# Optimization experiments

Hardware: AMD Instinct MI355X
Metric: run time of the kernel (lower is better)

The kernel has to match this reference:

```python
import jax, jax.numpy as jnp
import numpy as np

B, C, N = 8, 256, 4096
CQK = C // 4  # 64
BN_EPS = 1e-5


def setup_inputs() -> dict:
    key = jax.random.key(0)
    ks = jax.random.split(key, 10)
    s = 1.0 / np.sqrt(C)
    return {
        "x": jax.random.normal(ks[0], (B, C, N), jnp.float32),
        "xyz": jax.random.normal(ks[1], (B, C, N), jnp.float32),
        # q_conv and k_conv share the same weight/bias in the original module
        "wqk": jax.random.uniform(ks[2], (CQK, C), jnp.float32, -s, s),
        "bqk": jax.random.uniform(ks[3], (CQK,), jnp.float32, -s, s),
        "wv": jax.random.uniform(ks[4], (C, C), jnp.float32, -s, s),
        "bv": jax.random.uniform(ks[5], (C,), jnp.float32, -s, s),
        "wt": jax.random.uniform(ks[6], (C, C), jnp.float32, -s, s),
        "bt": jax.random.uniform(ks[7], (C,), jnp.float32, -s, s),
        "bn_gamma": jnp.ones((C,), jnp.float32),
        "bn_beta": jnp.zeros((C,), jnp.float32),
        "bn_mean": jax.random.normal(ks[8], (C,), jnp.float32) * 0.1,
        "bn_var": jax.random.uniform(ks[9], (C,), jnp.float32, 0.5, 1.5),
    }


def _conv1x1(x, w, b):
    # x: [B, Cin, N], w: [Cout, Cin], b: [Cout] -> [B, Cout, N]
    return jnp.einsum('oc,bcn->bon', w, x) + b[None, :, None]


def reference(x, xyz, wqk, bqk, wv, bv, wt, bt, bn_gamma, bn_beta, bn_mean, bn_var):
    x = x + xyz
    q = _conv1x1(x, wqk, bqk)            # [B, 64, N]
    k = _conv1x1(x, wqk, bqk)            # [B, 64, N] (shared weights)
    v = _conv1x1(x, wv, bv)              # [B, C, N]
    energy = jnp.einsum('bci,bcj->bij', q, k)   # q^T k -> [B, N, N]
    attn = jax.nn.softmax(energy, axis=-1)
    attn = attn / (1e-9 + attn.sum(axis=1, keepdims=True))  # L1 column renorm
    x_r = jnp.einsum('bcn,bnm->bcm', v, attn)    # [B, C, N]
    t = _conv1x1(x - x_r, wt, bt)
    # BatchNorm1d (eval mode, running stats)
    inv = jax.lax.rsqrt(bn_var + BN_EPS)
    t = (t - bn_mean[None, :, None]) * (inv * bn_gamma)[None, :, None] + bn_beta[None, :, None]
    x_r = jnp.where(t >= 0, t, 0.2 * t)          # LeakyReLU(0.2)
    return x + x_r
```

## Files before the change

### kernel.cpp

```cpp
#include <hip/hip_runtime.h>
#include <math.h>

#define B_   8
#define C_   256
#define N_   4096
#define CQK_ 64
#define JS_  8
#define NSPLIT 2
#define NRANGE (N_ / NSPLIT)

#define SCQ 1.20110674f
#define THR2 11.54f

typedef __attribute__((ext_vector_type(8))) short short8v;
typedef __attribute__((ext_vector_type(4))) short short4v;
typedef __attribute__((ext_vector_type(4))) float f32x4;
typedef __attribute__((ext_vector_type(16))) float f32x16;
typedef __attribute__((ext_vector_type(4))) unsigned int uint4v;

__device__ __forceinline__ unsigned short f2bf(float f) {
    unsigned u = __float_as_uint(f);
    u += 0x7fffu + ((u >> 16) & 1u);
    return (unsigned short)(u >> 16);
}
__device__ __forceinline__ float bf2f(unsigned short h) {
    return __uint_as_float((unsigned)h << 16);
}


__global__ __launch_bounds__(256) void wcvt_kernel(const float* __restrict__ wqk,
                                                   const float* __restrict__ wv,
                                                   const float* __restrict__ wt,
                                                   unsigned short* __restrict__ wh) {
    int i = (blockIdx.x * 256 + threadIdx.x) * 4;
    const float* src; int off;
    if (i < 16384)      { src = wqk; off = i; }
    else if (i < 81920) { src = wv;  off = i - 16384; }
    else                { src = wt;  off = i - 81920; }
    float4 v = *(const float4*)(src + off);
    short4v o;
    o[0] = (short)f2bf(v.x); o[1] = (short)f2bf(v.y);
    o[2] = (short)f2bf(v.z); o[3] = (short)f2bf(v.w);
    *(short4v*)(wh + i) = o;
}

__global__ __launch_bounds__(256) void addt_kernel(const float* __restrict__ x,
                                                   const float* __restrict__ xyz,
                                                   float* __restrict__ xs,
                                                   unsigned short* __restrict__ xst) {
    __shared__ float st[64][65];
    const int tid = threadIdx.x;
    const int n0 = blockIdx.x * 64, c0 = blockIdx.y * 64, b = blockIdx.z;
    const size_t base = ((size_t)b * C_ + c0) * N_ + n0;
#pragma unroll
    for (int r = 0; r < 4; ++r) {
        int c = r * 16 + (tid >> 4);
        int nc = (tid & 15) * 4;
        size_t off = base + (size_t)c * N_ + nc;
        float4 xv = *(const float4*)(x + off);
        float4 yv = *(const float4*)(xyz + off);
        float4 s = make_float4(xv.x + yv.x, xv.y + yv.y, xv.z + yv.z, xv.w + yv.w);
        *(float4*)(xs + off) = s;
        st[c][nc] = s.x; st[c][nc + 1] = s.y; st[c][nc + 2] = s.z; st[c][nc + 3] = s.w;
    }
    __syncthreads();
    int n = tid >> 2, cc = (tid & 3) * 16;
    short8v p0, p1;
#pragma unroll
    for (int j = 0; j < 8; ++j) {
        p0[j] = (short)f2bf(st[cc + j][n]);
        p1[j] = (short)f2bf(st[cc + 8 + j][n]);
    }
    size_t ob = ((size_t)b * N_ + n0 + n) * 256 + c0 + cc;
    *(short8v*)(xst + ob) = p0;
    *(short8v*)(xst + ob + 8) = p1;
}

__global__ __launch_bounds__(256, 4) void convq_kernel(const unsigned short* __restrict__ xst,
                                                       const unsigned short* __restrict__ wh,
                                                       const float* __restrict__ bias,
                                                       unsigned short* __restrict__ Qf) {
    const int tid = threadIdx.x, wave = tid >> 6, lane = tid & 63, q = lane & 15, g = lane >> 4;
    const int n0 = blockIdx.x * 64, b = blockIdx.y;
    const unsigned short* xb = xst + (size_t)b * N_ * 256;
    f32x4 acc[4];
#pragma unroll
    for (int j = 0; j < 4; ++j) acc[j] = (f32x4){0.f, 0.f, 0.f, 0.f};
    for (int ks = 0; ks < 8; ++ks) {
        short8v aw = *(const short8v*)(wh + (size_t)(wave * 16 + q) * 256 + ks * 32 + 8 * g);
#pragma unroll
        for (int j = 0; j < 4; ++j) {
            short8v bx = *(const short8v*)(xb + (size_t)(n0 + j * 16 + q) * 256 + ks * 32 + 8 * g);
            acc[j] = __builtin_amdgcn_mfma_f32_16x16x32_bf16(aw, bx, acc[j], 0, 0, 0);
        }
    }
#pragma unroll
    for (int j = 0; j < 4; ++j) {
        short4v pk;
#pragma unroll
        for (int r = 0; r < 4; ++r)
            pk[r] = (short)f2bf((acc[j][r] + bias[wave * 16 + 4 * g + r]) * SCQ);
        const int n = n0 + j * 16 + q;
        size_t a = ((((size_t)b * 128 + (n >> 5)) * 4 + wave) * 64 + (g >> 1) * 32 + (n & 31)) * 8
                   + (g & 1) * 4;
        *(short4v*)(Qf + a) = pk;
    }
}

__global__ __launch_bounds__(512, 2) void convv_kernel(const unsigned short* __restrict__ xst,
                                                       const unsigned short* __restrict__ wh,
                                                       const float* __restrict__ bias,
                                                       const float* __restrict__ rsinv,
                                                       unsigned short* __restrict__ Vf) {
    const int tid = threadIdx.x, wave = tid >> 6, lane = tid & 63, q = lane & 15, g = lane >> 4;
    const int n0 = blockIdx.x * 64, o0 = blockIdx.y * 128, b = blockIdx.z;
    const int oo = o0 + wave * 16;
    const unsigned short* xb = xst + (size_t)b * N_ * 256;
    const float* rsb = rsinv + (size_t)b * N_;
    f32x4 acc[4];
#pragma unroll
    for (int j = 0; j < 4; ++j) acc[j] = (f32x4){0.f, 0.f, 0.f, 0.f};
    for (int ks = 0; ks < 8; ++ks) {
        short8v bw = *(const short8v*)(wh + (size_t)(oo + q) * 256 + ks * 32 + 8 * g);
#pragma unroll
        for (int j = 0; j < 4; ++j) {
            short8v ax = *(const short8v*)(xb + (size_t)(n0 + j * 16 + q) * 256 + ks * 32 + 8 * g);
            acc[j] = __builtin_amdgcn_mfma_f32_16x16x32_bf16(ax, bw, acc[j], 0, 0, 0);
        }
    }
    float bo = bias[oo + q];
    const int c = oo + q;
#pragma unroll
    for (int j = 0; j < 4; ++j) {
        f32x4 rs4 = *(const f32x4*)(rsb + n0 + j * 16 + 4 * g);
        short4v pk;
#pragma unroll
        for (int r = 0; r < 4; ++r) pk[r] = (short)f2bf((acc[j][r] + bo) * rs4[r]);
        size_t a = ((((size_t)b * 256 + (n0 >> 4) + j) * 8 + (c >> 5)) * 64
                    + (g >> 1) * 32 + (c & 31)) * 8 + (g & 1) * 4;
        *(short4v*)(Vf + a) = pk;
    }
}

__global__ __launch_bounds__(256) void rowstats_mfma(const unsigned short* __restrict__ Qf,
                                                     float* __restrict__ pmax,
                                                     float* __restrict__ psum) {
    const int tid = threadIdx.x;
    const int wave = tid >> 6, lane = tid & 63, l31 = lane & 31;
    const int bid = blockIdx.x;
    const int b  = bid & 7;
    const int it = (bid >> 3) & 31;
    const int js = bid >> 8;
    const int i0 = it * 128 + wave * 32;
    const unsigned short* Qb = Qf + (size_t)b * 128 * 4 * 512;

    short8v bqi[4];
#pragma unroll
    for (int ks = 0; ks < 4; ++ks)
        bqi[ks] = *(const short8v*)(Qb + (((size_t)(i0 >> 5) * 4 + ks) * 64 + lane) * 8);

    float m = -1e30f, s = 0.f;
    const int jbeg = js * (N_ / JS_);
    for (int j0 = jbeg; j0 < jbeg + N_ / JS_; j0 += 32) {
        short8v an[4];
#pragma unroll
        for (int ks = 0; ks < 4; ++ks)
            an[ks] = *(const short8v*)(Qb + (((size_t)(j0 >> 5) * 4 + ks) * 64 + lane) * 8);
        f32x16 e;
#pragma unroll
        for (int r = 0; r < 16; ++r) e[r] = 0.f;
#pragma unroll
        for (int ks = 0; ks < 4; ++ks)
            e = __builtin_amdgcn_mfma_f32_32x32x16_bf16(an[ks], bqi[ks], e, 0, 0, 0);
        float pm = e[0];
#pragma unroll
        for (int r = 1; r < 16; ++r) pm = fmaxf(pm, e[r]);
        if (!__all(pm <= m + THR2)) {
            float mn = fmaxf(m, pm);
            s *= exp2f(m - mn);
            m = mn;
        }
#pragma unroll
        for (int r = 0; r < 16; ++r) s += exp2f(e[r] - m);
    }
    {
        float mo = __shfl_xor(m, 32);
        float so = __shfl_xor(s, 32);
        float mn = fmaxf(m, mo);
        s = s * exp2f(m - mn) + so * exp2f(mo - mn);
        m = mn;
    }
    if (lane < 32) {
        size_t o = ((size_t)js * B_ + b) * N_ + i0 + l31;
        pmax[o] = m;
        psum[o] = s;
    }
}

__global__ __launch_bounds__(256) void rowmerge_kernel(const float* __restrict__ pmax,
                                                       const float* __restrict__ psum,
                                                       float* __restrict__ rmneg,
                                                       float* __restrict__ rsinv) {
    size_t i = (size_t)blockIdx.x * 256 + threadIdx.x;
    float m = -1e30f;
#pragma unroll
    for (int js = 0; js < JS_; ++js) m = fmaxf(m, pmax[(size_t)js * B_ * N_ + i]);
    float s = 0.f;
#pragma unroll
    for (int js = 0; js < JS_; ++js)
        s += psum[(size_t)js * B_ * N_ + i] * exp2f(pmax[(size_t)js * B_ * N_ + i] - m);
    rmneg[i] = -m;
    rsinv[i] = 1.f / s;
}

__global__ __launch_bounds__(256, 2) void pv_mfma32(const unsigned short* __restrict__ Qf,
                                                    const unsigned short* __restrict__ Vf,
                                                    const float* __restrict__ rmneg,
                                                    const float* __restrict__ rsinv,
                                                    unsigned short* __restrict__ pxr,
                                                    float* __restrict__ pcs) {
    const int tid = threadIdx.x;
    const int wave = tid >> 6, lane = tid & 63, l31 = lane & 31, hi = lane >> 5;
    const int bid = blockIdx.x;
    const int b  = bid & 7;
    const int mc = (bid >> 3) & 31;
    const int ns = bid >> 8;
    const int m0 = mc * 128 + wave * 32;
    const int nbeg = ns * NRANGE;
    const unsigned short* Qb = Qf + (size_t)b * 128 * 4 * 512;
    const unsigned short* Vb = Vf + (size_t)b * 256 * 8 * 512;
    const float* rmb = rmneg + (size_t)b * N_;
    const float* rsb = rsinv + (size_t)b * N_;

    short8v bqm[4];
#pragma unroll
    for (int ks = 0; ks < 4; ++ks)
        bqm[ks] = *(const short8v*)(Qb + (((size_t)(m0 >> 5) * 4 + ks) * 64 + lane) * 8);

    f32x16 acc[8];
#pragma unroll
    for (int cb = 0; cb < 8; ++cb)
#pragma unroll
        for (int r = 0; r < 16; ++r) acc[cb][r] = 0.f;
    f32x4 csum4 = {0.f, 0.f, 0.f, 0.f};

#pragma unroll 1
    for (int it = 0; it < NRANGE / 32; ++it) {
        const int n0 = nbeg + it * 32;
        const int nt = n0 >> 5;
        short8v an[4];
#pragma unroll
        for (int ks = 0; ks < 4; ++ks)
            an[ks] = *(const short8v*)(Qb + (((size_t)nt * 4 + ks) * 64 + lane) * 8);
        f32x4 rmn[4], rs[4];
#pragma unroll
        for (int s = 0; s < 4; ++s) {
            rmn[s] = *(const f32x4*)(rmb + n0 + 8 * s + 4 * hi);
            rs[s]  = *(const f32x4*)(rsb + n0 + 8 * s + 4 * hi);
        }
        f32x16 e;
#pragma unroll
        for (int s = 0; s < 4; ++s) {
            e[4 * s + 0] = rmn[s][0]; e[4 * s + 1] = rmn[s][1];
            e[4 * s + 2] = rmn[s][2]; e[4 * s + 3] = rmn[s][3];
        }
#pragma unroll
        for (int ks = 0; ks < 4; ++ks)
            e = __builtin_amdgcn_mfma_f32_32x32x16_bf16(an[ks], bqm[ks], e, 0, 0, 0);
        unsigned dw[8];
#pragma unroll
        for (int s = 0; s < 4; ++s) {
            float p0 = exp2f(e[4 * s + 0]);
            float p1 = exp2f(e[4 * s + 1]);
            float p2 = exp2f(e[4 * s + 2]);
            float p3 = exp2f(e[4 * s + 3]);
            csum4[s] += (p0 * rs[s][0] + p1 * rs[s][1]) + (p2 * rs[s][2] + p3 * rs[s][3]);
            asm("v_cvt_pk_bf16_f32 %0, %1, %2" : "=v"(dw[2 * s + 0]) : "v"(p0), "v"(p1));
            asm("v_cvt_pk_bf16_f32 %0, %1, %2" : "=v"(dw[2 * s + 1]) : "v"(p2), "v"(p3));
        }
        asm("v_permlane32_swap_b32 %0, %1" : "+v"(dw[0]), "+v"(dw[2]));
        asm("v_permlane32_swap_b32 %0, %1" : "+v"(dw[1]), "+v"(dw[3]));
        asm("v_permlane32_swap_b32 %0, %1" : "+v"(dw[4]), "+v"(dw[6]));
        asm("v_permlane32_swap_b32 %0, %1" : "+v"(dw[5]), "+v"(dw[7]));
        uint4v t0 = {dw[0], dw[1], dw[2], dw[3]};
        uint4v t1 = {dw[4], dw[5], dw[6], dw[7]};
        short8v pf0 = __builtin_bit_cast(short8v, t0);
        short8v pf1 = __builtin_bit_cast(short8v, t1);
        const size_t vb0 = (size_t)(nt * 2) * 8;
#pragma unroll
        for (int cb = 0; cb < 8; ++cb) {
            short8v v0 = *(const short8v*)(Vb + ((vb0 + cb) * 64 + lane) * 8);
            acc[cb] = __builtin_amdgcn_mfma_f32_32x32x16_bf16(v0, pf0, acc[cb], 0, 0, 0);
        }
#pragma unroll
        for (int cb = 0; cb < 8; ++cb) {
            short8v v1 = *(const short8v*)(Vb + ((vb0 + 8 + cb) * 64 + lane) * 8);
            acc[cb] = __builtin_amdgcn_mfma_f32_32x32x16_bf16(v1, pf1, acc[cb], 0, 0, 0);
        }
    }

    float csum = (csum4[0] + csum4[1]) + (csum4[2] + csum4[3]);
    csum += __shfl_xor(csum, 32);
    if (lane < 32) pcs[((size_t)ns * B_ + b) * N_ + m0 + lane] = csum;
    unsigned short* pb = pxr + ((size_t)ns * B_ + b) * N_ * 256;
    const int m = m0 + l31;
#pragma unroll
    for (int cb = 0; cb < 8; ++cb)
#pragma unroll
        for (int s = 0; s < 4; ++s) {
            short4v pk;
#pragma unroll
            for (int r = 0; r < 4; ++r) pk[r] = (short)f2bf(acc[cb][4 * s + r]);
            *(short4v*)(pb + (size_t)m * 256 + cb * 32 + 8 * s + 4 * hi) = pk;
        }
}

__global__ __launch_bounds__(256) void reduce_diff(const unsigned short* __restrict__ pxr,
                                                   const float* __restrict__ pcs,
                                                   unsigned short* __restrict__ dh) {
    size_t i = (size_t)blockIdx.x * 256 + threadIdx.x;
    size_t e0 = i * 8;
    int m = (int)((e0 >> 8) & (N_ - 1));
    int b = (int)(e0 >> 20);
    float cs = pcs[(size_t)b * N_ + m] + pcs[((size_t)B_ + b) * N_ + m];
    float inv = 1.f / (1e-9f + cs);
    short8v p0 = *(const short8v*)(pxr + e0);
    short8v p1 = *(const short8v*)(pxr + (size_t)B_ * N_ * 256 + e0);
    short8v xv = *(const short8v*)(dh + e0);
    short8v o;
#pragma unroll
    for (int j = 0; j < 8; ++j) {
        float xr = (bf2f((unsigned short)p0[j]) + bf2f((unsigned short)p1[j])) * inv;
        o[j] = (short)f2bf(bf2f((unsigned short)xv[j]) - xr);
    }
    *(short8v*)(dh + e0) = o;
}

__global__ __launch_bounds__(512, 2) void convt_kernel(const unsigned short* __restrict__ dh,
                                                       const unsigned short* __restrict__ wh,
                                                       const float* __restrict__ bt,
                                                       const float* __restrict__ xs,
                                                       float* __restrict__ out,
                                                       const float* __restrict__ gam,
                                                       const float* __restrict__ bet,
                                                       const float* __restrict__ mu,
                                                       const float* __restrict__ var) {
    const int tid = threadIdx.x, wave = tid >> 6, lane = tid & 63, q = lane & 15, g = lane >> 4;
    const int m0 = blockIdx.x * 64, c0 = blockIdx.y * 128, b = blockIdx.z;
    const int cc = c0 + wave * 16;
    const unsigned short* db = dh + (size_t)b * N_ * 256;
    f32x4 acc[4];
#pragma unroll
    for (int j = 0; j < 4; ++j) acc[j] = (f32x4){0.f, 0.f, 0.f, 0.f};
    for (int ks = 0; ks < 8; ++ks) {
        short8v bw = *(const short8v*)(wh + (size_t)(cc + q) * 256 + ks * 32 + 8 * g);
#pragma unroll
        for (int j = 0; j < 4; ++j) {
            short8v ad = *(const short8v*)(db + (size_t)(m0 + j * 16 + q) * 256 + ks * 32 + 8 * g);
            acc[j] = __builtin_amdgcn_mfma_f32_16x16x32_bf16(ad, bw, acc[j], 0, 0, 0);
        }
    }
    const int c = cc + q;
    const float sc = rsqrtf(var[c] + 1e-5f) * gam[c];
    const float sh = bet[c] - mu[c] * sc;
    const float bb = bt[c];
#pragma unroll
    for (int j = 0; j < 4; ++j) {
        size_t off = ((size_t)b * C_ + c) * N_ + m0 + j * 16 + 4 * g;
        float4 xv = *(const float4*)(xs + off);
        float4 o;
        float tn;
        tn = (acc[j][0] + bb) * sc + sh; o.x = xv.x + (tn >= 0.f ? tn : 0.2f * tn);
        tn = (acc[j][1] + bb) * sc + sh; o.y = xv.y + (tn >= 0.f ? tn : 0.2f * tn);
        tn = (acc[j][2] + bb) * sc + sh; o.z = xv.z + (tn >= 0.f ? tn : 0.2f * tn);
        tn = (acc[j][3] + bb) * sc + sh; o.w = xv.w + (tn >= 0.f ? tn : 0.2f * tn);
        *(float4*)(out + off) = o;
    }
}

extern "C" void kernel_launch(void* const* d_in, const int* in_sizes, int n_in,
                              void* d_out, int out_size, void* d_ws, size_t ws_size,
                              hipStream_t stream) {
    (void)in_sizes; (void)n_in; (void)out_size; (void)ws_size;
    const float* x   = (const float*)d_in[0];
    const float* xyz = (const float*)d_in[1];
    const float* wqk = (const float*)d_in[2];
    const float* bqk = (const float*)d_in[3];
    const float* wv  = (const float*)d_in[4];
    const float* bv  = (const float*)d_in[5];
    const float* wt  = (const float*)d_in[6];
    const float* bt  = (const float*)d_in[7];
    const float* gam = (const float*)d_in[8];
    const float* bet = (const float*)d_in[9];
    const float* mu  = (const float*)d_in[10];
    const float* var = (const float*)d_in[11];
    float* out = (float*)d_out;

    const size_t M8 = (size_t)B_ * C_ * N_;
    float* ws = (float*)d_ws;
    size_t off = 0;
    float* xs = ws + off;                              off += M8;
    unsigned short* xst = (unsigned short*)(ws + off); off += M8 / 2;
    unsigned short* Qf  = (unsigned short*)(ws + off); off += M8 / 8;
    unsigned short* Vf  = (unsigned short*)(ws + off); off += M8 / 2;
    unsigned short* wh  = (unsigned short*)(ws + off); off += 81920;
    float* pmax = ws + off; off += (size_t)JS_ * B_ * N_;
    float* psum = ws + off; off += (size_t)JS_ * B_ * N_;
    float* rmb  = ws + off; off += (size_t)B_ * N_;
    float* rsb  = ws + off; off += (size_t)B_ * N_;
    float* pcs  = ws + off; off += (size_t)NSPLIT * B_ * N_;
    unsigned short* pxr = (unsigned short*)(ws + off); off += M8;
    unsigned short* dhb = xst;

    wcvt_kernel<<<dim3(144), dim3(256), 0, stream>>>(wqk, wv, wt, wh);
    addt_kernel<<<dim3(N_ / 64, C_ / 64, B_), dim3(256), 0, stream>>>(x, xyz, xs, xst);
    convq_kernel<<<dim3(N_ / 64, B_), dim3(256), 0, stream>>>(xst, wh, bqk, Qf);
    rowstats_mfma<<<dim3(B_ * 32 * JS_), dim3(256), 0, stream>>>(Qf, pmax, psum);
    rowmerge_kernel<<<dim3(B_ * N_ / 256), dim3(256), 0, stream>>>(pmax, psum, rmb, rsb);
    convv_kernel<<<dim3(N_ / 64, C_ / 128, B_), dim3(512), 0, stream>>>(
        xst, wh + 16384, bv, rsb, Vf);
    pv_mfma32<<<dim3(B_ * 32 * NSPLIT), dim3(256), 0, stream>>>(Qf, Vf, rmb, rsb, pxr, pcs);
    reduce_diff<<<dim3(B_ * N_ * C_ / 8 / 256), dim3(256), 0, stream>>>(pxr, pcs, dhb);
    convt_kernel<<<dim3(N_ / 64, C_ / 128, B_), dim3(512), 0, stream>>>(
        dhb, wh + 81920, bt, xs, out, gam, bet, mu, var);
}
```

Measured before the change: 301.9 us.

## Process two 32-column m tiles per wave in PV kernel to reuse V loads

Each wave in the PV attention kernel now computes two 32-wide output column tiles instead of one, so every V fragment and every Q row tile it loads feeds two MFMA accumulator sets. The grid is halved to 256 blocks and launch bounds drop to one block per SIMD group, which doubles accumulator register use (two sets of 8 f32x16). The aim is to halve global/L2 traffic for V and Q per unit of work. In exchange, occupancy falls, there are fewer blocks to fill the GPU, and register pressure may cause spills.

Result: slower. 517.0 us (+71.2%).

```diff
diff --git a/kernel.cpp b/kernel.cpp
--- a/kernel.cpp
+++ b/kernel.cpp
@@ -213,7 +213,7 @@
     rsinv[i] = 1.f / s;
 }
 
-__global__ __launch_bounds__(256, 2) void pv_mfma32(const unsigned short* __restrict__ Qf,
+__global__ __launch_bounds__(256, 1) void pv_mfma32(const unsigned short* __restrict__ Qf,
                                                     const unsigned short* __restrict__ Vf,
                                                     const float* __restrict__ rmneg,
                                                     const float* __restrict__ rsinv,
@@ -223,26 +223,28 @@
     const int wave = tid >> 6, lane = tid & 63, l31 = lane & 31, hi = lane >> 5;
     const int bid = blockIdx.x;
     const int b  = bid & 7;
-    const int mc = (bid >> 3) & 31;
-    const int ns = bid >> 8;
-    const int m0 = mc * 128 + wave * 32;
+    const int mc = (bid >> 3) & 15;
+    const int ns = bid >> 7;
+    const int m0 = mc * 256 + wave * 64;
     const int nbeg = ns * NRANGE;
     const unsigned short* Qb = Qf + (size_t)b * 128 * 4 * 512;
     const unsigned short* Vb = Vf + (size_t)b * 256 * 8 * 512;
     const float* rmb = rmneg + (size_t)b * N_;
     const float* rsb = rsinv + (size_t)b * N_;
 
-    short8v bqm[4];
-#pragma unroll
-    for (int ks = 0; ks < 4; ++ks)
-        bqm[ks] = *(const short8v*)(Qb + (((size_t)(m0 >> 5) * 4 + ks) * 64 + lane) * 8);
-
-    f32x16 acc[8];
+    short8v bqmA[4], bqmB[4];
+#pragma unroll
+    for (int ks = 0; ks < 4; ++ks) {
+        bqmA[ks] = *(const short8v*)(Qb + (((size_t)(m0 >> 5) * 4 + ks) * 64 + lane) * 8);
+        bqmB[ks] = *(const short8v*)(Qb + (((size_t)((m0 + 32) >> 5) * 4 + ks) * 64 + lane) * 8);
+    }
+
+    f32x16 accA[8], accB[8];
 #pragma unroll
     for (int cb = 0; cb < 8; ++cb)
 #pragma unroll
-        for (int r = 0; r < 16; ++r) acc[cb][r] = 0.f;
-    f32x4 csum4 = {0.f, 0.f, 0.f, 0.f};
+        for (int r = 0; r < 16; ++r) { accA[cb][r] = 0.f; accB[cb][r] = 0.f; }
+    f32x4 csA = {0.f, 0.f, 0.f, 0.f}, csB = {0.f, 0.f, 0.f, 0.f};
 
 #pragma unroll 1
     for (int it = 0; it < NRANGE / 32; ++it) {
@@ -258,60 +260,83 @@
             rmn[s] = *(const f32x4*)(rmb + n0 + 8 * s + 4 * hi);
             rs[s]  = *(const f32x4*)(rsb + n0 + 8 * s + 4 * hi);
         }
-        f32x16 e;
+        f32x16 eA, eB;
+#pragma unroll
+        for (int s = 0; s < 4; ++s)
+#pragma unroll
+            for (int r = 0; r < 4; ++r) { eA[4 * s + r] = rmn[s][r]; eB[4 * s + r] = rmn[s][r]; }
+#pragma unroll
+        for (int ks = 0; ks < 4; ++ks) {
+            eA = __builtin_amdgcn_mfma_f32_32x32x16_bf16(an[ks], bqmA[ks], eA, 0, 0, 0);
+            eB = __builtin_amdgcn_mfma_f32_32x32x16_bf16(an[ks], bqmB[ks], eB, 0, 0, 0);
+        }
+        unsigned dwA[8], dwB[8];
 #pragma unroll
         for (int s = 0; s < 4; ++s) {
-            e[4 * s + 0] = rmn[s][0]; e[4 * s + 1] = rmn[s][1];
-            e[4 * s + 2] = rmn[s][2]; e[4 * s + 3] = rmn[s][3];
-        }
-#pragma unroll
-        for (int ks = 0; ks < 4; ++ks)
-            e = __builtin_amdgcn_mfma_f32_32x32x16_bf16(an[ks], bqm[ks], e, 0, 0, 0);
-        unsigned dw[8];
-#pragma unroll
-        for (int s = 0; s < 4; ++s) {
-            float p0 = exp2f(e[4 * s + 0]);
-            float p1 = exp2f(e[4 * s + 1]);
-            float p2 = exp2f(e[4 * s + 2]);
-            float p3 = exp2f(e[4 * s + 3]);
-            csum4[s] += (p0 * rs[s][0] + p1 * rs[s][1]) + (p2 * rs[s][2] + p3 * rs[s][3]);
-            asm("v_cvt_pk_bf16_f32 %0, %1, %2" : "=v"(dw[2 * s + 0]) : "v"(p0), "v"(p1));
-            asm("v_cvt_pk_bf16_f32 %0, %1, %2" : "=v"(dw[2 * s + 1]) : "v"(p2), "v"(p3));
-        }
-        asm("v_permlane32_swap_b32 %0, %1" : "+v"(dw[0]), "+v"(dw[2]));
-        asm("v_permlane32_swap_b32 %0, %1" : "+v"(dw[1]), "+v"(dw[3]));
-        asm("v_permlane32_swap_b32 %0, %1" : "+v"(dw[4]), "+v"(dw[6]));
-        asm("v_permlane32_swap_b32 %0, %1" : "+v"(dw[5]), "+v"(dw[7]));
-        uint4v t0 = {dw[0], dw[1], dw[2], dw[3]};
-        uint4v t1 = {dw[4], dw[5], dw[6], dw[7]};
-        short8v pf0 = __builtin_bit_cast(short8v, t0);
-        short8v pf1 = __builtin_bit_cast(short8v, t1);
+            float a0 = exp2f(eA[4 * s + 0]), a1 = exp2f(eA[4 * s + 1]);
+            float a2 = exp2f(eA[4 * s + 2]), a3 = exp2f(eA[4 * s + 3]);
+            float b0 = exp2f(eB[4 * s + 0]), b1 = exp2f(eB[4 * s + 1]);
+            float b2 = exp2f(eB[4 * s + 2]), b3 = exp2f(eB[4 * s + 3]);
+            csA[s] += (a0 * rs[s][0] + a1 * rs[s][1]) + (a2 * rs[s][2] + a3 * rs[s][3]);
+            csB[s] += (b0 * rs[s][0] + b1 * rs[s][1]) + (b2 * rs[s][2] + b3 * rs[s][3]);
+            asm("v_cvt_pk_bf16_f32 %0, %1, %2" : "=v"(dwA[2 * s + 0]) : "v"(a0), "v"(a1));
+            asm("v_cvt_pk_bf16_f32 %0, %1, %2" : "=v"(dwA[2 * s + 1]) : "v"(a2), "v"(a3));
+            asm("v_cvt_pk_bf16_f32 %0, %1, %2" : "=v"(dwB[2 * s + 0]) : "v"(b0), "v"(b1));
+            asm("v_cvt_pk_bf16_f32 %0, %1, %2" : "=v"(dwB[2 * s + 1]) : "v"(b2), "v"(b3));
+        }
+        asm("v_permlane32_swap_b32 %0, %1" : "+v"(dwA[0]), "+v"(dwA[2]));
+        asm("v_permlane32_swap_b32 %0, %1" : "+v"(dwA[1]), "+v"(dwA[3]));
+        asm("v_permlane32_swap_b32 %0, %1" : "+v"(dwA[4]), "+v"(dwA[6]));
+        asm("v_permlane32_swap_b32 %0, %1" : "+v"(dwA[5]), "+v"(dwA[7]));
+        asm("v_permlane32_swap_b32 %0, %1" : "+v"(dwB[0]), "+v"(dwB[2]));
+        asm("v_permlane32_swap_b32 %0, %1" : "+v"(dwB[1]), "+v"(dwB[3]));
+        asm("v_permlane32_swap_b32 %0, %1" : "+v"(dwB[4]), "+v"(dwB[6]));
+        asm("v_permlane32_swap_b32 %0, %1" : "+v"(dwB[5]), "+v"(dwB[7]));
+        uint4v tA0 = {dwA[0], dwA[1], dwA[2], dwA[3]};
+        uint4v tA1 = {dwA[4], dwA[5], dwA[6], dwA[7]};
+        uint4v tB0 = {dwB[0], dwB[1], dwB[2], dwB[3]};
+        uint4v tB1 = {dwB[4], dwB[5], dwB[6], dwB[7]};
+        short8v pfA0 = __builtin_bit_cast(short8v, tA0);
+        short8v pfA1 = __builtin_bit_cast(short8v, tA1);
+        short8v pfB0 = __builtin_bit_cast(short8v, tB0);
+        short8v pfB1 = __builtin_bit_cast(short8v, tB1);
         const size_t vb0 = (size_t)(nt * 2) * 8;
 #pragma unroll
         for (int cb = 0; cb < 8; ++cb) {
             short8v v0 = *(const short8v*)(Vb + ((vb0 + cb) * 64 + lane) * 8);
-            acc[cb] = __builtin_amdgcn_mfma_f32_32x32x16_bf16(v0, pf0, acc[cb], 0, 0, 0);
+            accA[cb] = __builtin_amdgcn_mfma_f32_32x32x16_bf16(v0, pfA0, accA[cb], 0, 0, 0);
+            accB[cb] = __builtin_amdgcn_mfma_f32_32x32x16_bf16(v0, pfB0, accB[cb], 0, 0, 0);
         }
 #pragma unroll
         for (int cb = 0; cb < 8; ++cb) {
             short8v v1 = *(const short8v*)(Vb + ((vb0 + 8 + cb) * 64 + lane) * 8);
-            acc[cb] = __builtin_amdgcn_mfma_f32_32x32x16_bf16(v1, pf1, acc[cb], 0, 0, 0);
-        }
-    }
-
-    float csum = (csum4[0] + csum4[1]) + (csum4[2] + csum4[3]);
-    csum += __shfl_xor(csum, 32);
-    if (lane < 32) pcs[((size_t)ns * B_ + b) * N_ + m0 + lane] = csum;
+            accA[cb] = __builtin_amdgcn_mfma_f32_32x32x16_bf16(v1, pfA1, accA[cb], 0, 0, 0);
+            accB[cb] = __builtin_amdgcn_mfma_f32_32x32x16_bf16(v1, pfB1, accB[cb], 0, 0, 0);
+        }
+    }
+
+    float csumA = (csA[0] + csA[1]) + (csA[2] + csA[3]);
+    float csumB = (csB[0] + csB[1]) + (csB[2] + csB[3]);
+    csumA += __shfl_xor(csumA, 32);
+    csumB += __shfl_xor(csumB, 32);
+    if (lane < 32) {
+        pcs[((size_t)ns * B_ + b) * N_ + m0 + l31] = csumA;
+        pcs[((size_t)ns * B_ + b) * N_ + m0 + 32 + l31] = csumB;
+    }
     unsigned short* pb = pxr + ((size_t)ns * B_ + b) * N_ * 256;
-    const int m = m0 + l31;
+    const int mA = m0 + l31, mB = m0 + 32 + l31;
 #pragma unroll
     for (int cb = 0; cb < 8; ++cb)
 #pragma unroll
         for (int s = 0; s < 4; ++s) {
-            short4v pk;
-#pragma unroll
-            for (int r = 0; r < 4; ++r) pk[r] = (short)f2bf(acc[cb][4 * s + r]);
-            *(short4v*)(pb + (size_t)m * 256 + cb * 32 + 8 * s + 4 * hi) = pk;
+            short4v pkA, pkB;
+#pragma unroll
+            for (int r = 0; r < 4; ++r) {
+                pkA[r] = (short)f2bf(accA[cb][4 * s + r]);
+                pkB[r] = (short)f2bf(accB[cb][4 * s + r]);
+            }
+            *(short4v*)(pb + (size_t)mA * 256 + cb * 32 + 8 * s + 4 * hi) = pkA;
+            *(short4v*)(pb + (size_t)mB * 256 + cb * 32 + 8 * s + 4 * hi) = pkB;
         }
 }
 
@@ -419,7 +444,7 @@
     rowmerge_kernel<<<dim3(B_ * N_ / 256), dim3(256), 0, stream>>>(pmax, psum, rmb, rsb);
     convv_kernel<<<dim3(N_ / 64, C_ / 128, B_), dim3(512), 0, stream>>>(
         xst, wh + 16384, bv, rsb, Vf);
-    pv_mfma32<<<dim3(B_ * 32 * NSPLIT), dim3(256), 0, stream>>>(Qf, Vf, rmb, rsb, pxr, pcs);
+    pv_mfma32<<<dim3(B_ * 16 * NSPLIT), dim3(256), 0, stream>>>(Qf, Vf, rmb, rsb, pxr, pcs);
     reduce_diff<<<dim3(B_ * N_ * C_ / 8 / 256), dim3(256), 0, stream>>>(pxr, pcs, dhb);
     convt_kernel<<<dim3(N_ / 64, C_ / 128, B_), dim3(512), 0, stream>>>(
         dhb, wh + 81920, bt, xs, out, gam, bet, mu, var);
```
